# Kernel optimization log

Measured on AMD Instinct MI355X. Metric: run time of the kernel, lower is better.

The kernel has to match this reference:

```python
import jax, jax.numpy as jnp
import numpy as np

B, T, C = 4, 1024, 1024
H, D = 16, 64            # num_heads, head_size = C // H
F = 4096                 # ffwd_size
L = 4                    # num_layers
VOCAB = 64               # input_size (activity vocab)
OUT = 65                 # output_size (acts + 1 duration)
LEN = 1024               # positional table length (block_size)


def _rmsnorm(x, g):
    eps = jnp.finfo(x.dtype).eps
    return x * jax.lax.rsqrt(jnp.mean(x * x, axis=-1, keepdims=True) + eps) * g


def setup_inputs() -> dict:
    key = jax.random.key(0)
    ks = jax.random.split(key, 16)
    std = 0.02
    acts = jax.random.randint(ks[0], (B, T), 0, VOCAB, dtype=jnp.int32)
    durations = jax.random.uniform(ks[1], (B, T), dtype=jnp.float32)
    emb_table = jax.random.normal(ks[2], (VOCAB, C - 1), dtype=jnp.float32) * std
    pos_table = jax.random.normal(ks[3], (LEN, C), dtype=jnp.float32) * std
    Wq = jax.random.normal(ks[4], (L, H, C, D), dtype=jnp.float32) * std
    Wk = jax.random.normal(ks[5], (L, H, C, D), dtype=jnp.float32) * std
    Wv = jax.random.normal(ks[6], (L, H, C, D), dtype=jnp.float32) * std
    Wo = jax.random.normal(ks[7], (L, C, C), dtype=jnp.float32) * std
    bo = jnp.zeros((L, C), dtype=jnp.float32)
    W1 = jax.random.normal(ks[8], (L, C, F), dtype=jnp.float32) * std
    b1 = jnp.zeros((L, F), dtype=jnp.float32)
    W2 = jax.random.normal(ks[9], (L, F, C), dtype=jnp.float32) * std
    b2 = jnp.zeros((L, C), dtype=jnp.float32)
    g1 = jnp.ones((L, C), dtype=jnp.float32)
    g2 = jnp.ones((L, C), dtype=jnp.float32)
    lm_W = jax.random.normal(ks[10], (C, OUT), dtype=jnp.float32) * std
    lm_b = jnp.zeros((OUT,), dtype=jnp.float32)
    return dict(acts=acts, durations=durations, emb_table=emb_table, pos_table=pos_table,
                Wq=Wq, Wk=Wk, Wv=Wv, Wo=Wo, bo=bo, W1=W1, b1=b1, W2=W2, b2=b2,
                g1=g1, g2=g2, lm_W=lm_W, lm_b=lm_b)


def reference(acts, durations, emb_table, pos_table, Wq, Wk, Wv, Wo, bo,
              W1, b1, W2, b2, g1, g2, lm_W, lm_b):
    # embedding: concat(act embedding [C-1], duration scalar) -> [B, T, C]
    x = jnp.concatenate([emb_table[acts], durations[..., None]], axis=-1)
    x = x + pos_table[:T]
    tril = jnp.tril(jnp.ones((T, T), dtype=bool))
    scale = D ** -0.5
    for l in range(L):
        h = _rmsnorm(x, g1[l])
        q = jnp.einsum('btc,hcd->bhtd', h, Wq[l])
        k = jnp.einsum('btc,hcd->bhtd', h, Wk[l])
        v = jnp.einsum('btc,hcd->bhtd', h, Wv[l])
        wei = jnp.einsum('bhtd,bhsd->bhts', q, k) * scale
        wei = jnp.where(tril, wei, -jnp.inf)
        wei = jax.nn.softmax(wei, axis=-1)
        o = jnp.einsum('bhts,bhsd->bhtd', wei, v)           # [B, H, T, D]
        o = o.transpose(0, 2, 1, 3).reshape(B, T, H * D)     # concat heads
        x = x + o @ Wo[l] + bo[l]
        h2 = _rmsnorm(x, g2[l])
        x = x + jax.nn.gelu(h2 @ W1[l] + b1[l], approximate=False) @ W2[l] + b2[l]
    logits = x @ lm_W + lm_b
    acts_logits, dur = logits[..., :OUT - 1], logits[..., OUT - 1:]
    acts_log_probs = jax.nn.log_softmax(acts_logits, axis=-1)
    log_dur = jnp.log(jax.nn.sigmoid(dur))
    return jnp.concatenate([acts_log_probs, log_dur], axis=-1)
```

## Files before the change

### kernel.cpp

```cpp
#include <hip/hip_runtime.h>

#define Bq 4
#define Tq 1024
#define Cq 1024
#define Hq 16
#define Dq 64
#define Fq 4096
#define Lq 4
#define BT (Bq*Tq)

typedef __attribute__((ext_vector_type(8))) __bf16 bf16x8;
typedef __attribute__((ext_vector_type(4))) float  floatx4;

__device__ __forceinline__ unsigned short f2bf(float f) {
  unsigned int u = __builtin_bit_cast(unsigned int, f);
  u = (u + 0x7FFFu + ((u >> 16) & 1u)) >> 16;
  return (unsigned short)u;
}

__device__ __forceinline__ void gld_lds16(const void* g, void* lds) {
  __builtin_amdgcn_global_load_lds(
      (const __attribute__((address_space(1))) unsigned int*)g,
      (__attribute__((address_space(3))) unsigned int*)lds, 16, 0, 0);
}

__global__ __launch_bounds__(256) void embed_kernel(
    const int* __restrict__ acts, const float* __restrict__ dur,
    const float* __restrict__ emb, const float* __restrict__ pos,
    float* __restrict__ x)
{
  int tok = blockIdx.x;
  int t = tok & (Tq-1);
  int a = acts[tok];
  const float* er = emb + (size_t)a * (Cq-1);
  const float* pr = pos + (size_t)t * Cq;
  float* xr = x + (size_t)tok * Cq;
  float dv = dur[tok];
  for (int c = threadIdx.x; c < Cq; c += 256) {
    float v = (c < Cq-1) ? er[c] : dv;
    xr[c] = v + pr[c];
  }
}

__global__ __launch_bounds__(256) void rmsnorm_kernel(
    const float* __restrict__ x, const float* __restrict__ g,
    unsigned short* __restrict__ h)
{
  int tok = blockIdx.x, tid = threadIdx.x;
  const float4* xr = (const float4*)(x + (size_t)tok * Cq);
  float4 v = xr[tid];
  float ss = v.x*v.x + v.y*v.y + v.z*v.z + v.w*v.w;
  #pragma unroll
  for (int s = 32; s >= 1; s >>= 1) ss += __shfl_xor(ss, s, 64);
  __shared__ float ws4[4];
  if ((tid & 63) == 0) ws4[tid >> 6] = ss;
  __syncthreads();
  float tot = ws4[0] + ws4[1] + ws4[2] + ws4[3];
  float r = rsqrtf(tot * (1.0f/(float)Cq) + 1.1920928955078125e-07f);
  float4 gv = ((const float4*)g)[tid];
  unsigned short o4[4] = { f2bf(v.x*r*gv.x), f2bf(v.y*r*gv.y),
                           f2bf(v.z*r*gv.z), f2bf(v.w*r*gv.w) };
  *(uint2*)(h + (size_t)tok*Cq + tid*4) = *(const uint2*)o4;
}

__global__ void transpose_cast_kernel(
    const float* __restrict__ in, unsigned short* __restrict__ out,
    int R, int Cc, int nb2, long long ostr1, long long ostr2)
{
  __shared__ float tile[32][33];
  int c0 = blockIdx.x * 32, r0 = blockIdx.y * 32;
  int tx = threadIdx.x, ty = threadIdx.y;
  int z = blockIdx.z;
  const float* ip = in + (size_t)z * R * Cc;
  #pragma unroll
  for (int i = 0; i < 32; i += 8)
    tile[ty+i][tx] = ip[(size_t)(r0+ty+i)*Cc + c0 + tx];
  __syncthreads();
  unsigned short* op = out + (size_t)(z / nb2) * ostr1 + (size_t)(z % nb2) * ostr2;
  #pragma unroll
  for (int i = 0; i < 32; i += 8)
    op[(size_t)(c0+ty+i)*R + r0 + tx] = f2bf(tile[tx][ty+i]);
}

template <int EPI>
__global__ __launch_bounds__(256)
void gemm_bt_kernel(const unsigned short* __restrict__ A, int lda,
                    const unsigned short* __restrict__ Bt, int ldb,
                    int KS,
                    unsigned short* __restrict__ outB, int ldc,
                    unsigned short* __restrict__ vT,
                    float* __restrict__ outF, int ldf,
                    const float* __restrict__ bias)
{
  __shared__ unsigned short lds_a[2*128*32];
  __shared__ unsigned short lds_b[2*128*32];
  int tid = threadIdx.x;
  int lane = tid & 63, wv = tid >> 6;
  int lane15 = lane & 15, laneh = lane >> 4;
  int m0 = blockIdx.y * 128, n0 = blockIdx.x * 128;
  int wm = wv & 1, wn = wv >> 1;

  floatx4 acc[4][4];
  #pragma unroll
  for (int i = 0; i < 4; i++)
    #pragma unroll
    for (int j = 0; j < 4; j++) acc[i][j] = (floatx4){0.f,0.f,0.f,0.f};

  int seg0 = (wv*2+0)*64 + lane;
  int seg1 = (wv*2+1)*64 + lane;
  int ra0 = seg0 >> 2, ca0 = ((seg0 & 3) ^ (ra0 & 3)) * 8;
  int ra1 = seg1 >> 2, ca1 = ((seg1 & 3) ^ (ra1 & 3)) * 8;
  const unsigned short* a_src0 = A  + (size_t)(m0+ra0)*lda + ca0;
  const unsigned short* a_src1 = A  + (size_t)(m0+ra1)*lda + ca1;
  const unsigned short* b_src0 = Bt + (size_t)(n0+ra0)*ldb + ca0;
  const unsigned short* b_src1 = Bt + (size_t)(n0+ra1)*ldb + ca1;
  unsigned short* a_dst0 = &lds_a[(wv*2+0)*512];
  unsigned short* a_dst1 = &lds_a[(wv*2+1)*512];
  unsigned short* b_dst0 = &lds_b[(wv*2+0)*512];
  unsigned short* b_dst1 = &lds_b[(wv*2+1)*512];

  int sx = (laneh ^ (lane15 & 3)) * 8;

  int kbeg = (EPI == 3) ? blockIdx.z * KS : 0;
  int nIter = KS >> 5;

  auto stage = [&](int k0, int buf) {
    int off = buf * 4096;
    gld_lds16(a_src0 + k0, a_dst0 + off);
    gld_lds16(a_src1 + k0, a_dst1 + off);
    gld_lds16(b_src0 + k0, b_dst0 + off);
    gld_lds16(b_src1 + k0, b_dst1 + off);
  };

  stage(kbeg, 0);
  int cur = 0;
  for (int it = 0; it < nIter; ++it) {
    __syncthreads();
    if (it + 1 < nIter) stage(kbeg + (it+1)*32, cur ^ 1);
    const unsigned short* la = &lds_a[cur*4096];
    const unsigned short* lb = &lds_b[cur*4096];
    bf16x8 af[4], bf[4];
    #pragma unroll
    for (int i = 0; i < 4; i++)
      af[i] = *(const bf16x8*)&la[(wm*64 + i*16 + lane15)*32 + sx];
    #pragma unroll
    for (int j = 0; j < 4; j++)
      bf[j] = *(const bf16x8*)&lb[(wn*64 + j*16 + lane15)*32 + sx];
    #pragma unroll
    for (int i = 0; i < 4; i++)
      #pragma unroll
      for (int j = 0; j < 4; j++)
        acc[i][j] = __builtin_amdgcn_mfma_f32_16x16x32_bf16(af[i], bf[j], acc[i][j], 0, 0, 0);
    cur ^= 1;
  }

  float* outFz = (EPI == 3) ? outF + (size_t)blockIdx.z * BT * Cq : outF;

  #pragma unroll
  for (int i = 0; i < 4; i++) {
    int row = m0 + wm*64 + i*16 + laneh*4;
    #pragma unroll
    for (int j = 0; j < 4; j++) {
      int col = n0 + wn*64 + j*16 + lane15;
      #pragma unroll
      for (int r = 0; r < 4; r++) {
        float v = acc[i][j][r];
        int rr = row + r;
        if constexpr (EPI == 0) {
          if (col < 2048) {
            outB[(size_t)rr*ldc + col] = f2bf(v);
          } else {
            int b = rr >> 10, t = rr & (Tq-1);
            int hd = col - 2048, hh = hd >> 6, d = hd & 63;
            vT[(((size_t)b*Hq + hh)*Dq + d)*Tq + t] = f2bf(v);
          }
        } else if constexpr (EPI == 1) {
          float z = v + bias[col];
          float u = 0.79788456080286536f * (z + 0.044715f * z*z*z);
          float t = 1.f - 2.f / (__expf(2.f*u) + 1.f);
          float gl = 0.5f * z * (1.f + t);
          outB[(size_t)rr*ldc + col] = f2bf(gl);
        } else if constexpr (EPI == 2) {
          outF[(size_t)rr*ldf + col] += v + bias[col];
        } else {
          outFz[(size_t)rr*ldf + col] = v;
        }
      }
    }
  }
}

__global__ __launch_bounds__(256) void splitk_reduce_kernel(
    const float* __restrict__ p, float* __restrict__ x,
    const float* __restrict__ bias)
{
  size_t o = ((size_t)blockIdx.x * 256 + threadIdx.x) * 4;
  float4 a = *(const float4*)(p + o);
  float4 b = *(const float4*)(p + (size_t)BT*Cq + o);
  float4 xv = *(const float4*)(x + o);
  float4 bi = *(const float4*)(bias + (o & (Cq-1)));
  xv.x += a.x + b.x + bi.x;
  xv.y += a.y + b.y + bi.y;
  xv.z += a.z + b.z + bi.z;
  xv.w += a.w + b.w + bi.w;
  *(float4*)(x + o) = xv;
}

__global__ __launch_bounds__(256)
void attn_kernel(const unsigned short* __restrict__ qk,
                 const unsigned short* __restrict__ vT,
                 unsigned short* __restrict__ ob)
{
  __shared__ unsigned short Ks [2][64*64];
  __shared__ unsigned short Vts[2][64*64];
  __shared__ unsigned short Ps [4*16*64];
  int tid = threadIdx.x, lane = tid & 63, wv = tid >> 6;
  int lane15 = lane & 15, laneh = lane >> 4;
  int blk = blockIdx.x;
  int p = blk & 7, bh = blk >> 3;
  int h = bh & (Hq-1), b = bh >> 4;
  size_t tokbase = (size_t)b * Tq;
  const unsigned short* Kbase = qk + tokbase*2048 + 1024 + h*64;
  const unsigned short* Vbase = vT + (size_t)bh * Dq * Tq;

  int so  = (laneh ^ (lane15 & 7)) * 8;
  int so32 = so ^ 32;
  unsigned short* Pw = &Ps[wv*1024];
  int pslot = ((laneh >> 1) ^ (lane15 & 7));

  auto stage = [&](int j0, int buf) {
    #pragma unroll
    for (int i = 0; i < 2; i++) {
      int seg = (wv*2+i)*64 + lane;
      int row = seg >> 3;
      int col = ((seg & 7) ^ (row & 7)) * 8;
      gld_lds16(Kbase + (size_t)(j0+row)*2048 + col, &Ks [buf][(wv*2+i)*512]);
      gld_lds16(Vbase + (size_t)row*Tq + j0 + col,   &Vts[buf][(wv*2+i)*512]);
    }
  };

  for (int phase = 0; phase < 2; ++phase) {
    int qt = phase ? (15 - p) : p;
    int qrow0 = qt*64 + wv*16;
    bf16x8 qf0, qf1;
    {
      const unsigned short* qp = qk + (tokbase + qrow0 + lane15)*2048 + h*64 + laneh*8;
      qf0 = *(const bf16x8*)(qp);
      qf1 = *(const bf16x8*)(qp + 32);
    }
    floatx4 oacc[4];
    #pragma unroll
    for (int d = 0; d < 4; d++) oacc[d] = (floatx4){0.f,0.f,0.f,0.f};
    float mrow = -__builtin_inff(), lrow = 0.f;
    int nT = qt + 1;

    __syncthreads();
    stage(0, 0);
    for (int it = 0; it < nT; ++it) {
      __syncthreads();
      if (it + 1 < nT) stage((it+1)*64, (it+1) & 1);
      int buf = it & 1;
      int j0 = it*64;

      floatx4 sac[4];
      #pragma unroll
      for (int jt = 0; jt < 4; jt++) {
        int row = jt*16 + lane15;
        bf16x8 kf0 = *(const bf16x8*)&Ks[buf][row*64 + so];
        bf16x8 kf1 = *(const bf16x8*)&Ks[buf][row*64 + so32];
        sac[jt] = (floatx4){0.f,0.f,0.f,0.f};
        sac[jt] = __builtin_amdgcn_mfma_f32_16x16x32_bf16(kf0, qf0, sac[jt], 0, 0, 0);
        sac[jt] = __builtin_amdgcn_mfma_f32_16x16x32_bf16(kf1, qf1, sac[jt], 0, 0, 0);
      }
      if (j0 + 63 > qrow0) {
        int tokg = qrow0 + lane15;
        #pragma unroll
        for (int jt = 0; jt < 4; jt++)
          #pragma unroll
          for (int r = 0; r < 4; r++) {
            int kv = j0 + jt*16 + laneh*4 + r;
            sac[jt][r] = (kv <= tokg) ? sac[jt][r] * 0.125f : -__builtin_inff();
          }
      } else {
        #pragma unroll
        for (int jt = 0; jt < 4; jt++)
          #pragma unroll
          for (int r = 0; r < 4; r++) sac[jt][r] *= 0.125f;
      }
      float mx = sac[0][0];
      #pragma unroll
      for (int jt = 0; jt < 4; jt++)
        #pragma unroll
        for (int r = 0; r < 4; r++) mx = fmaxf(mx, sac[jt][r]);
      mx = fmaxf(mx, __shfl_xor(mx, 16, 64));
      mx = fmaxf(mx, __shfl_xor(mx, 32, 64));
      float mn = fmaxf(mrow, mx);
      float alpha = __expf(mrow - mn);
      float psum = 0.f;
      #pragma unroll
      for (int jt = 0; jt < 4; jt++)
        #pragma unroll
        for (int r = 0; r < 4; r++) {
          float pv = __expf(sac[jt][r] - mn);
          sac[jt][r] = pv;
          psum += pv;
        }
      psum += __shfl_xor(psum, 16, 64);
      psum += __shfl_xor(psum, 32, 64);
      lrow = lrow * alpha + psum;
      mrow = mn;
      #pragma unroll
      for (int dt = 0; dt < 4; dt++)
        #pragma unroll
        for (int r = 0; r < 4; r++) oacc[dt][r] *= alpha;

      #pragma unroll
      for (int jt = 0; jt < 4; jt++) {
        unsigned int p0 = (unsigned int)f2bf(sac[jt][0]) | ((unsigned int)f2bf(sac[jt][1]) << 16);
        unsigned int p1 = (unsigned int)f2bf(sac[jt][2]) | ((unsigned int)f2bf(sac[jt][3]) << 16);
        int slot = (jt*2 + (laneh >> 1)) ^ (lane15 & 7);
        *(uint2*)&Pw[lane15*64 + slot*8 + (laneh & 1)*4] = make_uint2(p0, p1);
      }
      bf16x8 pf0 = *(const bf16x8*)&Pw[lane15*64 + so];
      bf16x8 pf1 = *(const bf16x8*)&Pw[lane15*64 + so32];
      #pragma unroll
      for (int dt = 0; dt < 4; dt++) {
        int row = dt*16 + lane15;
        bf16x8 vf0 = *(const bf16x8*)&Vts[buf][row*64 + so];
        bf16x8 vf1 = *(const bf16x8*)&Vts[buf][row*64 + so32];
        oacc[dt] = __builtin_amdgcn_mfma_f32_16x16x32_bf16(vf0, pf0, oacc[dt], 0, 0, 0);
        oacc[dt] = __builtin_amdgcn_mfma_f32_16x16x32_bf16(vf1, pf1, oacc[dt], 0, 0, 0);
      }
    }
    float inv = 1.f / lrow;
    unsigned short* orow = ob + (tokbase + qrow0 + lane15)*Cq + h*64 + laneh*4;
    #pragma unroll
    for (int dt = 0; dt < 4; dt++) {
      unsigned int u0 = (unsigned int)f2bf(oacc[dt][0]*inv) | ((unsigned int)f2bf(oacc[dt][1]*inv) << 16);
      unsigned int u1 = (unsigned int)f2bf(oacc[dt][2]*inv) | ((unsigned int)f2bf(oacc[dt][3]*inv) << 16);
      *(uint2*)&orow[dt*16] = make_uint2(u0, u1);
    }
  }
}

__global__ __launch_bounds__(256) void lmw_prep_kernel(
    const float* __restrict__ lmW, unsigned short* __restrict__ lmWt,
    float* __restrict__ lmWcol)
{
  int idx = blockIdx.x * 256 + threadIdx.x;
  int n = idx & 63, k = idx >> 6;
  lmWt[(size_t)n*Cq + k] = f2bf(lmW[(size_t)k*65 + n]);
  if (idx < Cq) lmWcol[idx] = lmW[(size_t)idx*65 + 64];
}

__global__ __launch_bounds__(64) void head_mfma_kernel(
    const float* __restrict__ x, const unsigned short* __restrict__ lmWt,
    const float* __restrict__ lmWcol, const float* __restrict__ lmb,
    float* __restrict__ out)
{
  int lane = threadIdx.x;
  int lane15 = lane & 15, laneh = lane >> 4;
  int tok0 = blockIdx.x * 16;

  floatx4 acc[4];
  #pragma unroll
  for (int jt = 0; jt < 4; jt++) acc[jt] = (floatx4){0.f,0.f,0.f,0.f};

  const float* xrow = x + (size_t)(tok0 + lane15) * Cq + laneh*8;
  const unsigned short* brow = lmWt + (size_t)lane15 * Cq + laneh*8;

  for (int k0 = 0; k0 < Cq; k0 += 32) {
    float4 a0 = *(const float4*)(xrow + k0);
    float4 a1 = *(const float4*)(xrow + k0 + 4);
    bf16x8 af;
    af[0] = (__bf16)a0.x; af[1] = (__bf16)a0.y; af[2] = (__bf16)a0.z; af[3] = (__bf16)a0.w;
    af[4] = (__bf16)a1.x; af[5] = (__bf16)a1.y; af[6] = (__bf16)a1.z; af[7] = (__bf16)a1.w;
    #pragma unroll
    for (int jt = 0; jt < 4; jt++) {
      bf16x8 bfv = *(const bf16x8*)(brow + (size_t)jt*16*Cq + k0);
      acc[jt] = __builtin_amdgcn_mfma_f32_16x16x32_bf16(af, bfv, acc[jt], 0, 0, 0);
    }
  }
  #pragma unroll
  for (int jt = 0; jt < 4; jt++) {
    float bias = lmb[jt*16 + lane15];
    #pragma unroll
    for (int r = 0; r < 4; r++) acc[jt][r] += bias;
  }
  #pragma unroll
  for (int r = 0; r < 4; r++) {
    float m = fmaxf(fmaxf(acc[0][r], acc[1][r]), fmaxf(acc[2][r], acc[3][r]));
    #pragma unroll
    for (int s = 1; s < 16; s <<= 1) m = fmaxf(m, __shfl_xor(m, s, 64));
    float se = 0.f;
    #pragma unroll
    for (int jt = 0; jt < 4; jt++) se += expf(acc[jt][r] - m);
    #pragma unroll
    for (int s = 1; s < 16; s <<= 1) se += __shfl_xor(se, s, 64);
    float lse = m + logf(se);
    int tok = tok0 + laneh*4 + r;
    float* orow = out + (size_t)tok * 65;
    #pragma unroll
    for (int jt = 0; jt < 4; jt++)
      orow[jt*16 + lane15] = acc[jt][r] - lse;
  }
  int t = lane >> 2, kq = (lane & 3) * 256;
  const float* xr2 = x + (size_t)(tok0 + t) * Cq + kq;
  const float* wc = lmWcol + kq;
  float s = 0.f;
  #pragma unroll 4
  for (int i = 0; i < 256; i += 4) {
    float4 xv = *(const float4*)(xr2 + i);
    float4 wv = *(const float4*)(wc + i);
    s += xv.x*wv.x + xv.y*wv.y + xv.z*wv.z + xv.w*wv.w;
  }
  s += __shfl_xor(s, 1, 64);
  s += __shfl_xor(s, 2, 64);
  if ((lane & 3) == 0) {
    float z = s + lmb[64];
    float ls = (z >= 0.f) ? -log1pf(expf(-z)) : (z - log1pf(expf(z)));
    out[(size_t)(tok0 + t) * 65 + 64] = ls;
  }
}

extern "C" void kernel_launch(void* const* d_in, const int* in_sizes, int n_in,
                              void* d_out, int out_size, void* d_ws, size_t ws_size,
                              hipStream_t stream) {
  const int*   acts = (const int*)  d_in[0];
  const float* dur  = (const float*)d_in[1];
  const float* emb  = (const float*)d_in[2];
  const float* pos  = (const float*)d_in[3];
  const float* Wq   = (const float*)d_in[4];
  const float* Wk   = (const float*)d_in[5];
  const float* Wv   = (const float*)d_in[6];
  const float* Wo   = (const float*)d_in[7];
  const float* bo   = (const float*)d_in[8];
  const float* W1   = (const float*)d_in[9];
  const float* b1   = (const float*)d_in[10];
  const float* W2   = (const float*)d_in[11];
  const float* b2   = (const float*)d_in[12];
  const float* g1   = (const float*)d_in[13];
  const float* g2   = (const float*)d_in[14];
  const float* lmW  = (const float*)d_in[15];
  const float* lmb  = (const float*)d_in[16];
  float* out = (float*)d_out;
  (void)in_sizes; (void)n_in; (void)out_size; (void)ws_size;

  char* w = (char*)d_ws;
  auto take = [&](size_t bytes) { char* p = w; w += (bytes + 255) & ~(size_t)255; return p; };
  unsigned short* qk  = (unsigned short*)take((size_t)BT*2048*2);
  unsigned short* vT  = (unsigned short*)take((size_t)Bq*Hq*Dq*Tq*2);
  unsigned short* ob  = (unsigned short*)take((size_t)BT*Cq*2);
  unsigned short* m1  = qk;
  unsigned short* hb  = (unsigned short*)take((size_t)BT*Cq*2);
  float*          x   = (float*)take((size_t)BT*Cq*4);
  unsigned short* wqkvl = (unsigned short*)take((size_t)3072*Cq*2);
  unsigned short* wol   = (unsigned short*)take((size_t)Cq*Cq*2);
  unsigned short* w1l   = (unsigned short*)take((size_t)Fq*Cq*2);
  unsigned short* w2l   = (unsigned short*)take((size_t)Cq*Fq*2);
  unsigned short* lmWt  = (unsigned short*)take((size_t)64*Cq*2);
  float*          lmWcol= (float*)take((size_t)Cq*4);
  float*          part  = (float*)take((size_t)2*BT*Cq*4);

  dim3 tb(32, 8);
  embed_kernel<<<BT, 256, 0, stream>>>(acts, dur, emb, pos, x);
  lmw_prep_kernel<<<256, 256, 0, stream>>>(lmW, lmWt, lmWcol);

  for (int l = 0; l < Lq; l++) {
    transpose_cast_kernel<<<dim3(2,32,16), tb, 0, stream>>>(
        Wq + (size_t)l*Hq*Cq*Dq, wqkvl,               1024, 64, 16, 0, (long long)64*1024);
    transpose_cast_kernel<<<dim3(2,32,16), tb, 0, stream>>>(
        Wk + (size_t)l*Hq*Cq*Dq, wqkvl + 1024*1024,   1024, 64, 16, 0, (long long)64*1024);
    transpose_cast_kernel<<<dim3(2,32,16), tb, 0, stream>>>(
        Wv + (size_t)l*Hq*Cq*Dq, wqkvl + 2048*1024,   1024, 64, 16, 0, (long long)64*1024);
    transpose_cast_kernel<<<dim3(32,32,1), tb, 0, stream>>>(
        Wo + (size_t)l*Cq*Cq,    wol,  1024, 1024, 1, 0, 0);
    transpose_cast_kernel<<<dim3(128,32,1), tb, 0, stream>>>(
        W1 + (size_t)l*Cq*Fq,    w1l,  1024, 4096, 1, 0, 0);
    transpose_cast_kernel<<<dim3(32,128,1), tb, 0, stream>>>(
        W2 + (size_t)l*Fq*Cq,    w2l,  4096, 1024, 1, 0, 0);

    rmsnorm_kernel<<<BT, 256, 0, stream>>>(x, g1 + l*Cq, hb);
    gemm_bt_kernel<0><<<dim3(24,32), 256, 0, stream>>>(
        hb, Cq, wqkvl, Cq, Cq, qk, 2048, vT, nullptr, 0, nullptr);
    attn_kernel<<<Bq*Hq*8, 256, 0, stream>>>(qk, vT, ob);
    gemm_bt_kernel<2><<<dim3(8,32), 256, 0, stream>>>(
        ob, Cq, wol, Cq, Cq, nullptr, 0, nullptr, x, Cq, bo + l*Cq);
    rmsnorm_kernel<<<BT, 256, 0, stream>>>(x, g2 + l*Cq, hb);
    gemm_bt_kernel<1><<<dim3(32,32), 256, 0, stream>>>(
        hb, Cq, w1l, Cq, Cq, m1, Fq, nullptr, nullptr, 0, b1 + l*Fq);
    gemm_bt_kernel<3><<<dim3(8,32,2), 256, 0, stream>>>(
        m1, Fq, w2l, Fq, 2048, nullptr, 0, nullptr, part, Cq, nullptr);
    splitk_reduce_kernel<<<BT*Cq/1024, 256, 0, stream>>>(part, x, b2 + l*Cq);
  }
  head_mfma_kernel<<<BT/16, 64, 0, stream>>>(x, lmWt, lmWcol, lmb, out);
}
```

Measured before the change: 1.258 ms.

## Triple-buffer GEMM LDS staging and merge weight transpose launches

The GEMM main loop moves from double to triple buffering of the LDS tiles. Loads are issued two k-steps ahead, and a partial vmcnt wait plus a barrier replaces the full __syncthreads, so global-to-LDS loads overlap more with MFMA work. Separately, the six per-layer weight transpose/cast launches are merged into one kernel that dispatches on block index, which cuts launch overhead. The cost is more LDS per block, which may lower occupancy, and correctness now depends on the hand-written waitcnt assumptions.

New measurement: 1.218 ms. -3.2%, faster.

```diff
diff --git a/kernel.cpp b/kernel.cpp
--- a/kernel.cpp
+++ b/kernel.cpp
@@ -22,6 +22,10 @@
   __builtin_amdgcn_global_load_lds(
       (const __attribute__((address_space(1))) unsigned int*)g,
       (__attribute__((address_space(3))) unsigned int*)lds, 16, 0, 0);
+}
+
+__device__ __forceinline__ void barrier_vmcnt4() {
+  asm volatile("s_waitcnt vmcnt(4)\n\ts_barrier" ::: "memory");
 }
 
 __global__ __launch_bounds__(256) void embed_kernel(
@@ -63,23 +67,47 @@
   *(uint2*)(h + (size_t)tok*Cq + tid*4) = *(const uint2*)o4;
 }
 
-__global__ void transpose_cast_kernel(
-    const float* __restrict__ in, unsigned short* __restrict__ out,
-    int R, int Cc, int nb2, long long ostr1, long long ostr2)
+__global__ void prep_layer_kernel(
+    const float* __restrict__ Wq, const float* __restrict__ Wk,
+    const float* __restrict__ Wv, const float* __restrict__ Wo,
+    const float* __restrict__ W1, const float* __restrict__ W2,
+    unsigned short* __restrict__ wqkvl, unsigned short* __restrict__ wol,
+    unsigned short* __restrict__ w1l,   unsigned short* __restrict__ w2l)
 {
   __shared__ float tile[32][33];
-  int c0 = blockIdx.x * 32, r0 = blockIdx.y * 32;
-  int tx = threadIdx.x, ty = threadIdx.y;
-  int z = blockIdx.z;
-  const float* ip = in + (size_t)z * R * Cc;
+  int z = blockIdx.x;
+  const float* in; unsigned short* out;
+  int R, Cc, tx, ty;
+  if (z < 3072) {
+    int i = z >> 10, t = z & 1023;
+    int hh = t >> 6, rem = t & 63;
+    ty = rem >> 1; tx = rem & 1;
+    const float* w = (i == 0) ? Wq : (i == 1) ? Wk : Wv;
+    in = w + (size_t)hh * Cq * Dq;
+    out = wqkvl + (size_t)i * 1024 * 1024 + (size_t)hh * 64 * 1024;
+    R = 1024; Cc = 64;
+  } else if (z < 4096) {
+    int t = z - 3072;
+    tx = t & 31; ty = t >> 5;
+    in = Wo; out = wol; R = 1024; Cc = 1024;
+  } else if (z < 8192) {
+    int t = z - 4096;
+    tx = t & 127; ty = t >> 7;
+    in = W1; out = w1l; R = 1024; Cc = 4096;
+  } else {
+    int t = z - 8192;
+    tx = t & 31; ty = t >> 5;
+    in = W2; out = w2l; R = 4096; Cc = 1024;
+  }
+  int c0 = tx * 32, r0 = ty * 32;
+  int lx = threadIdx.x, ly = threadIdx.y;
   #pragma unroll
   for (int i = 0; i < 32; i += 8)
-    tile[ty+i][tx] = ip[(size_t)(r0+ty+i)*Cc + c0 + tx];
+    tile[ly+i][lx] = in[(size_t)(r0+ly+i)*Cc + c0 + lx];
   __syncthreads();
-  unsigned short* op = out + (size_t)(z / nb2) * ostr1 + (size_t)(z % nb2) * ostr2;
   #pragma unroll
   for (int i = 0; i < 32; i += 8)
-    op[(size_t)(c0+ty+i)*R + r0 + tx] = f2bf(tile[tx][ty+i]);
+    out[(size_t)(c0+ly+i)*R + r0 + lx] = f2bf(tile[lx][ly+i]);
 }
 
 template <int EPI>
@@ -92,8 +120,8 @@
                     float* __restrict__ outF, int ldf,
                     const float* __restrict__ bias)
 {
-  __shared__ unsigned short lds_a[2*128*32];
-  __shared__ unsigned short lds_b[2*128*32];
+  __shared__ unsigned short lds_a[3*4096];
+  __shared__ unsigned short lds_b[3*4096];
   int tid = threadIdx.x;
   int lane = tid & 63, wv = tid >> 6;
   int lane15 = lane & 15, laneh = lane >> 4;
@@ -133,12 +161,13 @@
   };
 
   stage(kbeg, 0);
-  int cur = 0;
+  stage(kbeg + 32, 1);
+  int cb = 0, pb = 2;
   for (int it = 0; it < nIter; ++it) {
-    __syncthreads();
-    if (it + 1 < nIter) stage(kbeg + (it+1)*32, cur ^ 1);
-    const unsigned short* la = &lds_a[cur*4096];
-    const unsigned short* lb = &lds_b[cur*4096];
+    barrier_vmcnt4();
+    if (it + 2 < nIter) stage(kbeg + (it+2)*32, pb);
+    const unsigned short* la = &lds_a[cb*4096];
+    const unsigned short* lb = &lds_b[cb*4096];
     bf16x8 af[4], bf[4];
     #pragma unroll
     for (int i = 0; i < 4; i++)
@@ -151,7 +180,8 @@
       #pragma unroll
       for (int j = 0; j < 4; j++)
         acc[i][j] = __builtin_amdgcn_mfma_f32_16x16x32_bf16(af[i], bf[j], acc[i][j], 0, 0, 0);
-    cur ^= 1;
+    cb = (cb == 2) ? 0 : cb + 1;
+    pb = (pb == 2) ? 0 : pb + 1;
   }
 
   float* outFz = (EPI == 3) ? outF + (size_t)blockIdx.z * BT * Cq : outF;
@@ -226,7 +256,6 @@
   int so  = (laneh ^ (lane15 & 7)) * 8;
   int so32 = so ^ 32;
   unsigned short* Pw = &Ps[wv*1024];
-  int pslot = ((laneh >> 1) ^ (lane15 & 7));
 
   auto stage = [&](int j0, int buf) {
     #pragma unroll
@@ -467,18 +496,10 @@
   lmw_prep_kernel<<<256, 256, 0, stream>>>(lmW, lmWt, lmWcol);
 
   for (int l = 0; l < Lq; l++) {
-    transpose_cast_kernel<<<dim3(2,32,16), tb, 0, stream>>>(
-        Wq + (size_t)l*Hq*Cq*Dq, wqkvl,               1024, 64, 16, 0, (long long)64*1024);
-    transpose_cast_kernel<<<dim3(2,32,16), tb, 0, stream>>>(
-        Wk + (size_t)l*Hq*Cq*Dq, wqkvl + 1024*1024,   1024, 64, 16, 0, (long long)64*1024);
-    transpose_cast_kernel<<<dim3(2,32,16), tb, 0, stream>>>(
-        Wv + (size_t)l*Hq*Cq*Dq, wqkvl + 2048*1024,   1024, 64, 16, 0, (long long)64*1024);
-    transpose_cast_kernel<<<dim3(32,32,1), tb, 0, stream>>>(
-        Wo + (size_t)l*Cq*Cq,    wol,  1024, 1024, 1, 0, 0);
-    transpose_cast_kernel<<<dim3(128,32,1), tb, 0, stream>>>(
-        W1 + (size_t)l*Cq*Fq,    w1l,  1024, 4096, 1, 0, 0);
-    transpose_cast_kernel<<<dim3(32,128,1), tb, 0, stream>>>(
-        W2 + (size_t)l*Fq*Cq,    w2l,  4096, 1024, 1, 0, 0);
+    prep_layer_kernel<<<12288, tb, 0, stream>>>(
+        Wq + (size_t)l*Hq*Cq*Dq, Wk + (size_t)l*Hq*Cq*Dq, Wv + (size_t)l*Hq*Cq*Dq,
+        Wo + (size_t)l*Cq*Cq, W1 + (size_t)l*Cq*Fq, W2 + (size_t)l*Fq*Cq,
+        wqkvl, wol, w1l, w2l);
 
     rmsnorm_kernel<<<BT, 256, 0, stream>>>(x, g1 + l*Cq, hb);
     gemm_bt_kernel<0><<<dim3(24,32), 256, 0, stream>>>(
```
